# Kernel optimization log

Measured on AMD Instinct MI355X. Metric: run time of the kernel, lower is better.

## Reference

```python
import jax, jax.numpy as jnp
import numpy as np

# Dimensions: SASA-style local self-attention, 7x7 window, 8 groups (heads)
B, CIN, H, W = 4, 256, 64, 64
COUT, K, PAD, STRIDE, DIL, G = 256, 7, 3, 1, 1, 8
CG = COUT // G  # channels per group


def setup_inputs() -> dict:
    key = jax.random.key(0)
    k1, k2, k3, k4, k5, k6 = jax.random.split(key, 6)
    s = 1.0 / np.sqrt(CIN // G)  # fan-in scaling like torch conv init
    return {
        "inputs": jax.random.normal(k1, (B, CIN, H, W), jnp.float32),
        "w_q": jax.random.normal(k2, (G, CG, CIN // G), jnp.float32) * s,
        "w_k": jax.random.normal(k3, (G, CG, CIN // G), jnp.float32) * s,
        "w_v": jax.random.normal(k4, (G, CG, CIN // G), jnp.float32) * s,
        "row_emb": jax.random.normal(k5, (COUT // 2, K), jnp.float32),
        "col_emb": jax.random.normal(k6, (COUT // 2, K), jnp.float32),
    }


def _proj(x, w):
    # grouped 1x1 conv: x [B,CIN,H,W], w [G, CG, CIN/G] -> [B,G,CG,H,W]
    xg = x.reshape(B, G, CIN // G, H, W)
    return jnp.einsum('goc,bgchw->bgohw', w, xg)


def _out_hw():
    ho = (H + 2 * PAD - DIL * (K - 1) - 1) // STRIDE + 1
    wo = (W + 2 * PAD - DIL * (K - 1) - 1) // STRIDE + 1
    return ho, wo


def _patches(x):
    # im2col matching torch.nn.Unfold ordering (kh slow, kw fast)
    # x [B,G,CG,H,W] -> [B,G,CG,K*K,Ho,Wo]
    ho, wo = _out_hw()
    xp = jnp.pad(x, ((0, 0), (0, 0), (0, 0), (PAD, PAD), (PAD, PAD)))
    pats = [
        xp[..., i * DIL: i * DIL + (ho - 1) * STRIDE + 1: STRIDE,
              j * DIL: j * DIL + (wo - 1) * STRIDE + 1: STRIDE]
        for i in range(K) for j in range(K)
    ]
    return jnp.stack(pats, axis=3)


def reference(inputs, w_q, w_k, w_v, row_emb, col_emb):
    ho, wo = _out_hw()
    # queries: 1x1 conv then unfold with kernel 1 / stride -> just strided subsample
    q = _proj(inputs, w_q)[..., ::STRIDE, ::STRIDE]          # [B,G,CG,Ho,Wo]
    kk = _patches(_proj(inputs, w_k))                         # [B,G,CG,K2,Ho,Wo]
    vv = _patches(_proj(inputs, w_v))                         # [B,G,CG,K2,Ho,Wo]
    # relative row/col embeddings, concatenated along channels, split per group
    emb_row = jnp.broadcast_to(row_emb[:, :, None], (COUT // 2, K, K))
    emb_col = jnp.broadcast_to(col_emb[:, None, :], (COUT // 2, K, K))
    emb = jnp.concatenate([emb_row, emb_col], axis=0).reshape(G, CG, K * K)
    # attention logits: per-position dot of query with (key + embedding)
    logits = jnp.einsum('bgchw,bgckhw->bgkhw', q, kk + emb[None, :, :, :, None, None])
    attn = jax.nn.softmax(logits, axis=2)                     # softmax over K*K window
    out = jnp.einsum('bgckhw,bgkhw->bgchw', vv, attn)
    return out.reshape(B, COUT, ho, wo)
```

## Files before the change

kernel.cpp:

```cpp
#include <hip/hip_runtime.h>
#include <hip/hip_bf16.h>
#include <hip/hip_fp16.h>

#define TS   16
#define HS   22
#define HP   484
#define KDW  18
#define KK   7
#define K2   49

typedef _Float16 h2   __attribute__((ext_vector_type(2)));
typedef _Float16 f16x8 __attribute__((ext_vector_type(8)));
typedef float    f32x4 __attribute__((ext_vector_type(4)));
union U32H { unsigned u; h2 h; __half2 p; };

__device__ __forceinline__ h2 pkrtz(float a, float b) {
    auto r = __builtin_amdgcn_cvt_pkrtz(a, b);
    union { decltype(r) i; h2 o; } c; c.i = r;
    return c.o;
}
__device__ __forceinline__ float dot2(h2 a, h2 b, float c) {
#if __has_builtin(__builtin_amdgcn_fdot2)
    return __builtin_amdgcn_fdot2(a, b, c, false);
#else
    return fmaf((float)a.x, (float)b.x, fmaf((float)a.y, (float)b.y, c));
#endif
}
__device__ __forceinline__ float dot2u(unsigned wu, h2 b, float c) {
    U32H w; w.u = wu; return dot2(w.h, b, c);
}
__device__ __forceinline__ float pswap(float v) {
#if __has_builtin(__builtin_amdgcn_mov_dpp)
    int j = __builtin_amdgcn_mov_dpp(__float_as_int(v), 0xB1, 0xF, 0xF, true);
    return __int_as_float(j);
#else
    return __shfl_xor(v, 1, 64);
#endif
}

__global__ __attribute__((amdgpu_flat_work_group_size(512, 512), amdgpu_waves_per_eu(4, 4)))
void sasa_fused_kernel(const float* __restrict__ x,
                       const float* __restrict__ wq,
                       const float* __restrict__ wk,
                       const float* __restrict__ wv,
                       const float* __restrict__ row_emb,
                       const float* __restrict__ col_emb,
                       float* __restrict__ out)
{
    __shared__ h2       s_w[1536];
    __shared__ float    s_emb[224];
    __shared__ unsigned s_ku[HP * KDW];
    __shared__ unsigned s_vu[HP * KDW];

    const int tid = threadIdx.x;

    const int lin  = blockIdx.x + (blockIdx.y << 2) + (blockIdx.z << 4);
    const int xcd  = lin & 7;
    const int slot = lin >> 3;
    const int zg   = xcd + ((slot >> 4) << 3);
    const int sp   = slot & 15;
    const int b    = zg >> 3;
    const int g    = zg & 7;
    const int y0   = (sp >> 2) * TS;
    const int x0   = (sp & 3) * TS;

    const float* xg = x + (size_t)(b * 256 + g * 32) * 4096;

    {
        const int cp  = tid & 15;
        const int cog = tid >> 4;
        const int hh  = cog >> 4;
        const int co  = cog & 15;
        const int di  = (hh * 16 + cp) * 16 + co;
        const float2* wk2 = (const float2*)(wk + g * 1024);
        const float2* wv2 = (const float2*)(wv + g * 1024);
        const float2* wq2 = (const float2*)(wq + g * 1024);
        float2 a = wk2[tid]; s_w[di]        = pkrtz(a.x, a.y);
        float2 v = wv2[tid]; s_w[512 + di]  = pkrtz(v.x, v.y);
        float2 q = wq2[tid]; s_w[1024 + di] = pkrtz(q.x, q.y);
    }
    if (tid < 224) {
        int c = tid / KK, t = tid - c * KK;
        s_emb[tid] = (g < 4) ? row_emb[(g * 32 + c) * KK + t]
                             : col_emb[((g - 4) * 32 + c) * KK + t];
    }
    __syncthreads();

    {
        const int lane = tid & 63;
        const int wid  = tid >> 6;
        const int lrow = lane & 15;
        const int lgrp = lane >> 4;

        f16x8 bk0, bk1, bv0, bv1;
        #pragma unroll
        for (int j = 0; j < 4; ++j) {
            const int cp = lgrp * 4 + j;
            h2 pk0 = s_w[(0 * 16 + cp) * 16 + lrow];
            h2 pk1 = s_w[(1 * 16 + cp) * 16 + lrow];
            h2 pv0 = s_w[512 + (0 * 16 + cp) * 16 + lrow];
            h2 pv1 = s_w[512 + (1 * 16 + cp) * 16 + lrow];
            bk0[2 * j] = pk0.x; bk0[2 * j + 1] = pk0.y;
            bk1[2 * j] = pk1.x; bk1[2 * j + 1] = pk1.y;
            bv0[2 * j] = pv0.x; bv0[2 * j + 1] = pv0.y;
            bv1[2 * j] = pv1.x; bv1[2 * j + 1] = pv1.y;
        }

        _Float16* sk16 = (_Float16*)s_ku;
        _Float16* sv16 = (_Float16*)s_vu;
        const f32x4 zero = {0.f, 0.f, 0.f, 0.f};

        #pragma unroll 1
        for (int t = wid; t < 31; t += 8) {
            const int hp = t * 16 + lrow;
            f16x8 a;
            bool valid = false;
            int gy = 0, gx = 0;
            if (hp < HP) {
                const int hy = hp / HS, hx = hp - hy * HS;
                gy = y0 + hy - 3; gx = x0 + hx - 3;
                valid = ((unsigned)gy < 64u) && ((unsigned)gx < 64u);
            }
            if (valid) {
                const float* xp = xg + gy * 64 + gx + (size_t)(lgrp * 8) * 4096;
                #pragma unroll
                for (int i2 = 0; i2 < 4; ++i2) {
                    h2 pr = pkrtz(xp[(2 * i2) * 4096], xp[(2 * i2 + 1) * 4096]);
                    a[2 * i2] = pr.x; a[2 * i2 + 1] = pr.y;
                }
            } else {
                #pragma unroll
                for (int i = 0; i < 8; ++i) a[i] = (_Float16)0.f;
            }

            f32x4 dk0 = __builtin_amdgcn_mfma_f32_16x16x32_f16(a, bk0, zero, 0, 0, 0);
            f32x4 dk1 = __builtin_amdgcn_mfma_f32_16x16x32_f16(a, bk1, zero, 0, 0, 0);
            f32x4 dv0 = __builtin_amdgcn_mfma_f32_16x16x32_f16(a, bv0, zero, 0, 0, 0);
            f32x4 dv1 = __builtin_amdgcn_mfma_f32_16x16x32_f16(a, bv1, zero, 0, 0, 0);

            #pragma unroll
            for (int r = 0; r < 4; ++r) {
                const int hpo = t * 16 + lgrp * 4 + r;
                if (hpo < HP) {
                    const int base = hpo * 36;
                    sk16[base + lrow]      = (_Float16)dk0[r];
                    sk16[base + 16 + lrow] = (_Float16)dk1[r];
                    sv16[base + lrow]      = (_Float16)dv0[r];
                    sv16[base + 16 + lrow] = (_Float16)dv1[r];
                }
            }
        }
    }

    const int p  = tid >> 1;
    const int h  = tid & 1;
    const int tx = p & 15, ty = p >> 4;
    const int yy = y0 + ty, xx = x0 + tx;
    float accQ[16];
    #pragma unroll
    for (int c = 0; c < 16; ++c) accQ[c] = 0.f;
    {
        const float* xp = xg + yy * 64 + xx;
        h2 xv2[16];
        #pragma unroll
        for (int cp = 0; cp < 16; ++cp)
            xv2[cp] = pkrtz(xp[(2 * cp) * 4096], xp[(2 * cp + 1) * 4096]);
        const h2* wqp = s_w + 1024 + h * 256;
        #pragma unroll
        for (int cp = 0; cp < 16; ++cp) {
            h2 xv = xv2[cp];
            const uint4* wqr = (const uint4*)(wqp + cp * 16);
            uint4 qw[4] = { wqr[0], wqr[1], wqr[2], wqr[3] };
            const unsigned* qwu = (const unsigned*)qw;
            #pragma unroll
            for (int co = 0; co < 16; ++co)
                accQ[co] = dot2u(qwu[co], xv, accQ[co]);
        }
    }

    float qe[KK];
    #pragma unroll
    for (int t = 0; t < KK; ++t) {
        float a = 0.f;
        #pragma unroll
        for (int c = 0; c < 16; ++c)
            a = fmaf(accQ[c], s_emb[(h * 16 + c) * KK + t], a);
        qe[t] = a + 0.f;
    }
    #pragma unroll
    for (int t = 0; t < KK; ++t)
        qe[t] += pswap(qe[t]);

    h2 q2[8];
    #pragma unroll
    for (int j = 0; j < 8; ++j) q2[j] = pkrtz(accQ[2 * j], accQ[2 * j + 1]);

    __syncthreads();

    const int rowsel = (g < 4) ? 1 : 0;

    float lg[K2];
    const unsigned* kb = s_ku + h * 8;
    #pragma unroll
    for (int tp = 0; tp < 24; ++tp) {
        const int t0 = 2 * tp, t1 = t0 + 1;
        const int ki0 = t0 / KK, kj0 = t0 - ki0 * KK;
        const int ki1 = t1 / KK, kj1 = t1 - ki1 * KK;
        const uint2* kp0 = (const uint2*)(kb + ((ty + ki0) * HS + tx + kj0) * KDW);
        const uint2* kp1 = (const uint2*)(kb + ((ty + ki1) * HS + tx + kj1) * KDW);
        uint2 a0 = kp0[0], a1 = kp0[1], a2 = kp0[2], a3 = kp0[3];
        uint2 b0 = kp1[0], b1 = kp1[1], b2 = kp1[2], b3 = kp1[3];
        float p0 = 0.f, p1 = 0.f;
        p0 = dot2u(a0.x, q2[0], p0);  p1 = dot2u(b0.x, q2[0], p1);
        p0 = dot2u(a0.y, q2[1], p0);  p1 = dot2u(b0.y, q2[1], p1);
        p0 = dot2u(a1.x, q2[2], p0);  p1 = dot2u(b1.x, q2[2], p1);
        p0 = dot2u(a1.y, q2[3], p0);  p1 = dot2u(b1.y, q2[3], p1);
        p0 = dot2u(a2.x, q2[4], p0);  p1 = dot2u(b2.x, q2[4], p1);
        p0 = dot2u(a2.y, q2[5], p0);  p1 = dot2u(b2.y, q2[5], p1);
        p0 = dot2u(a3.x, q2[6], p0);  p1 = dot2u(b3.x, q2[6], p1);
        p0 = dot2u(a3.y, q2[7], p0);  p1 = dot2u(b3.y, q2[7], p1);
        lg[t0] = p0 + pswap(p0) + (rowsel ? qe[ki0] : qe[kj0]);
        lg[t1] = p1 + pswap(p1) + (rowsel ? qe[ki1] : qe[kj1]);
    }
    {
        const uint2* kp = (const uint2*)(kb + ((ty + 6) * HS + tx + 6) * KDW);
        uint2 a0 = kp[0], a1 = kp[1], a2 = kp[2], a3 = kp[3];
        float p0 = 0.f;
        p0 = dot2u(a0.x, q2[0], p0); p0 = dot2u(a0.y, q2[1], p0);
        p0 = dot2u(a1.x, q2[2], p0); p0 = dot2u(a1.y, q2[3], p0);
        p0 = dot2u(a2.x, q2[4], p0); p0 = dot2u(a2.y, q2[5], p0);
        p0 = dot2u(a3.x, q2[6], p0); p0 = dot2u(a3.y, q2[7], p0);
        lg[48] = p0 + pswap(p0) + qe[6];
    }

    float m0 = lg[0], m1 = lg[1], m2 = lg[2], m3 = lg[3];
    #pragma unroll
    for (int t = 4; t < 48; t += 4) {
        m0 = fmaxf(m0, lg[t]);
        m1 = fmaxf(m1, lg[t + 1]);
        m2 = fmaxf(m2, lg[t + 2]);
        m3 = fmaxf(m3, lg[t + 3]);
    }
    const float mx = fmaxf(fmaxf(m0, m1), fmaxf(m2, fmaxf(m3, lg[48])));

    float s0 = 0.f, s1 = 0.f, s2 = 0.f, s3 = 0.f;
    #pragma unroll
    for (int t = 0; t < K2; ++t) {
        float pe = __expf(lg[t] - mx);
        lg[t] = pe;
        if ((t & 3) == 0) s0 += pe;
        else if ((t & 3) == 1) s1 += pe;
        else if ((t & 3) == 2) s2 += pe;
        else s3 += pe;
    }
    const float s = (s0 + s1) + (s2 + s3);

    __half2 o2[8];
    #pragma unroll
    for (int j = 0; j < 8; ++j) o2[j] = __float2half2_rn(0.f);

    const unsigned* vb = s_vu + h * 8;
    #pragma unroll
    for (int tp = 0; tp < 24; ++tp) {
        const int t0 = 2 * tp, t1 = t0 + 1;
        const int ki0 = t0 / KK, kj0 = t0 - ki0 * KK;
        const int ki1 = t1 / KK, kj1 = t1 - ki1 * KK;
        const uint2* vp0 = (const uint2*)(vb + ((ty + ki0) * HS + tx + kj0) * KDW);
        const uint2* vp1 = (const uint2*)(vb + ((ty + ki1) * HS + tx + kj1) * KDW);
        uint2 a0 = vp0[0], a1 = vp0[1], a2 = vp0[2], a3 = vp0[3];
        uint2 b0 = vp1[0], b1 = vp1[1], b2 = vp1[2], b3 = vp1[3];
        const __half2 pe0 = __float2half2_rn(lg[t0]);
        const __half2 pe1 = __float2half2_rn(lg[t1]);
        U32H c0, c1, c2, c3, c4, c5, c6, c7;
        c0.u = a0.x; c1.u = a0.y; c2.u = a1.x; c3.u = a1.y;
        c4.u = a2.x; c5.u = a2.y; c6.u = a3.x; c7.u = a3.y;
        o2[0] = __hfma2(c0.p, pe0, o2[0]);
        o2[1] = __hfma2(c1.p, pe0, o2[1]);
        o2[2] = __hfma2(c2.p, pe0, o2[2]);
        o2[3] = __hfma2(c3.p, pe0, o2[3]);
        o2[4] = __hfma2(c4.p, pe0, o2[4]);
        o2[5] = __hfma2(c5.p, pe0, o2[5]);
        o2[6] = __hfma2(c6.p, pe0, o2[6]);
        o2[7] = __hfma2(c7.p, pe0, o2[7]);
        c0.u = b0.x; c1.u = b0.y; c2.u = b1.x; c3.u = b1.y;
        c4.u = b2.x; c5.u = b2.y; c6.u = b3.x; c7.u = b3.y;
        o2[0] = __hfma2(c0.p, pe1, o2[0]);
        o2[1] = __hfma2(c1.p, pe1, o2[1]);
        o2[2] = __hfma2(c2.p, pe1, o2[2]);
        o2[3] = __hfma2(c3.p, pe1, o2[3]);
        o2[4] = __hfma2(c4.p, pe1, o2[4]);
        o2[5] = __hfma2(c5.p, pe1, o2[5]);
        o2[6] = __hfma2(c6.p, pe1, o2[6]);
        o2[7] = __hfma2(c7.p, pe1, o2[7]);
    }
    {
        const uint2* vp = (const uint2*)(vb + ((ty + 6) * HS + tx + 6) * KDW);
        uint2 a0 = vp[0], a1 = vp[1], a2 = vp[2], a3 = vp[3];
        const __half2 pe0 = __float2half2_rn(lg[48]);
        U32H c0, c1, c2, c3, c4, c5, c6, c7;
        c0.u = a0.x; c1.u = a0.y; c2.u = a1.x; c3.u = a1.y;
        c4.u = a2.x; c5.u = a2.y; c6.u = a3.x; c7.u = a3.y;
        o2[0] = __hfma2(c0.p, pe0, o2[0]);
        o2[1] = __hfma2(c1.p, pe0, o2[1]);
        o2[2] = __hfma2(c2.p, pe0, o2[2]);
        o2[3] = __hfma2(c3.p, pe0, o2[3]);
        o2[4] = __hfma2(c4.p, pe0, o2[4]);
        o2[5] = __hfma2(c5.p, pe0, o2[5]);
        o2[6] = __hfma2(c6.p, pe0, o2[6]);
        o2[7] = __hfma2(c7.p, pe0, o2[7]);
    }

    const float inv = 1.0f / s;
    float* op = out + (size_t)(b * 256 + g * 32 + h * 16) * 4096 + yy * 64 + xx;
    #pragma unroll
    for (int j = 0; j < 8; ++j) {
        float2 f = __half22float2(o2[j]);
        op[(2 * j) * 4096]     = f.x * inv;
        op[(2 * j + 1) * 4096] = f.y * inv;
    }
}

extern "C" void kernel_launch(void* const* d_in, const int* in_sizes, int n_in,
                              void* d_out, int out_size, void* d_ws, size_t ws_size,
                              hipStream_t stream) {
    const float* x       = (const float*)d_in[0];
    const float* wq      = (const float*)d_in[1];
    const float* wk      = (const float*)d_in[2];
    const float* wv      = (const float*)d_in[3];
    const float* row_emb = (const float*)d_in[4];
    const float* col_emb = (const float*)d_in[5];
    float* out = (float*)d_out;

    dim3 grid(4, 4, 32);
    dim3 block(512);
    sasa_fused_kernel<<<grid, block, 0, stream>>>(x, wq, wk, wv, row_emb, col_emb, out);
}
```

Measured before the change: 40.06 us.

## Share one LDS buffer for K and V, staging V in registers

Replaces the separate key and value LDS tiles with a single shared buffer. The V projection results are held in registers (packed half2) while logits are computed from K, then written into the same buffer after a barrier, followed by a second barrier before the weighted sum. Halving LDS use, together with relaxing waves_per_eu to 4–8, is meant to let two 512-thread blocks fit per CU. The cost is two extra block-wide barriers and 16 extra live registers per thread across the logit phase.

New measurement: 46.00 us. 14.8% more time.

```diff
diff --git a/kernel.cpp b/kernel.cpp
--- a/kernel.cpp
+++ b/kernel.cpp
@@ -38,7 +38,7 @@
 #endif
 }
 
-__global__ __attribute__((amdgpu_flat_work_group_size(512, 512), amdgpu_waves_per_eu(4, 4)))
+__global__ __attribute__((amdgpu_flat_work_group_size(512, 512), amdgpu_waves_per_eu(4, 8)))
 void sasa_fused_kernel(const float* __restrict__ x,
                        const float* __restrict__ wq,
                        const float* __restrict__ wk,
@@ -49,8 +49,7 @@
 {
     __shared__ h2       s_w[1536];
     __shared__ float    s_emb[224];
-    __shared__ unsigned s_ku[HP * KDW];
-    __shared__ unsigned s_vu[HP * KDW];
+    __shared__ unsigned s_kv[HP * KDW];
 
     const int tid = threadIdx.x;
 
@@ -86,12 +85,13 @@
     }
     __syncthreads();
 
-    {
-        const int lane = tid & 63;
-        const int wid  = tid >> 6;
-        const int lrow = lane & 15;
-        const int lgrp = lane >> 4;
-
+    const int lane = tid & 63;
+    const int wid  = tid >> 6;
+    const int lrow = lane & 15;
+    const int lgrp = lane >> 4;
+    unsigned vv[4][4];
+
+    {
         f16x8 bk0, bk1, bv0, bv1;
         #pragma unroll
         for (int j = 0; j < 4; ++j) {
@@ -106,48 +106,53 @@
             bv1[2 * j] = pv1.x; bv1[2 * j + 1] = pv1.y;
         }
 
-        _Float16* sk16 = (_Float16*)s_ku;
-        _Float16* sv16 = (_Float16*)s_vu;
+        _Float16* sk16 = (_Float16*)s_kv;
         const f32x4 zero = {0.f, 0.f, 0.f, 0.f};
 
-        #pragma unroll 1
-        for (int t = wid; t < 31; t += 8) {
-            const int hp = t * 16 + lrow;
-            f16x8 a;
-            bool valid = false;
-            int gy = 0, gx = 0;
-            if (hp < HP) {
-                const int hy = hp / HS, hx = hp - hy * HS;
-                gy = y0 + hy - 3; gx = x0 + hx - 3;
-                valid = ((unsigned)gy < 64u) && ((unsigned)gx < 64u);
-            }
-            if (valid) {
-                const float* xp = xg + gy * 64 + gx + (size_t)(lgrp * 8) * 4096;
+        #pragma unroll
+        for (int it = 0; it < 4; ++it) {
+            const int t = wid + it * 8;
+            if (t < 31) {
+                const int hp = t * 16 + lrow;
+                f16x8 a;
+                bool valid = false;
+                int gy = 0, gx = 0;
+                if (hp < HP) {
+                    const int hy = hp / HS, hx = hp - hy * HS;
+                    gy = y0 + hy - 3; gx = x0 + hx - 3;
+                    valid = ((unsigned)gy < 64u) && ((unsigned)gx < 64u);
+                }
+                if (valid) {
+                    const float* xp = xg + gy * 64 + gx + (size_t)(lgrp * 8) * 4096;
+                    #pragma unroll
+                    for (int i2 = 0; i2 < 4; ++i2) {
+                        h2 pr = pkrtz(xp[(2 * i2) * 4096], xp[(2 * i2 + 1) * 4096]);
+                        a[2 * i2] = pr.x; a[2 * i2 + 1] = pr.y;
+                    }
+                } else {
+                    #pragma unroll
+                    for (int i = 0; i < 8; ++i) a[i] = (_Float16)0.f;
+                }
+
+                f32x4 dk0 = __builtin_amdgcn_mfma_f32_16x16x32_f16(a, bk0, zero, 0, 0, 0);
+                f32x4 dk1 = __builtin_amdgcn_mfma_f32_16x16x32_f16(a, bk1, zero, 0, 0, 0);
+                f32x4 dv0 = __builtin_amdgcn_mfma_f32_16x16x32_f16(a, bv0, zero, 0, 0, 0);
+                f32x4 dv1 = __builtin_amdgcn_mfma_f32_16x16x32_f16(a, bv1, zero, 0, 0, 0);
+
                 #pragma unroll
-                for (int i2 = 0; i2 < 4; ++i2) {
-                    h2 pr = pkrtz(xp[(2 * i2) * 4096], xp[(2 * i2 + 1) * 4096]);
-                    a[2 * i2] = pr.x; a[2 * i2 + 1] = pr.y;
+                for (int r = 0; r < 4; ++r) {
+                    const int hpo = t * 16 + lgrp * 4 + r;
+                    U32H pv; pv.h = pkrtz(dv0[r], dv1[r]);
+                    vv[it][r] = pv.u;
+                    if (hpo < HP) {
+                        const int base = hpo * 36;
+                        sk16[base + lrow]      = (_Float16)dk0[r];
+                        sk16[base + 16 + lrow] = (_Float16)dk1[r];
+                    }
                 }
             } else {
                 #pragma unroll
-                for (int i = 0; i < 8; ++i) a[i] = (_Float16)0.f;
-            }
-
-            f32x4 dk0 = __builtin_amdgcn_mfma_f32_16x16x32_f16(a, bk0, zero, 0, 0, 0);
-            f32x4 dk1 = __builtin_amdgcn_mfma_f32_16x16x32_f16(a, bk1, zero, 0, 0, 0);
-            f32x4 dv0 = __builtin_amdgcn_mfma_f32_16x16x32_f16(a, bv0, zero, 0, 0, 0);
-            f32x4 dv1 = __builtin_amdgcn_mfma_f32_16x16x32_f16(a, bv1, zero, 0, 0, 0);
-
-            #pragma unroll
-            for (int r = 0; r < 4; ++r) {
-                const int hpo = t * 16 + lgrp * 4 + r;
-                if (hpo < HP) {
-                    const int base = hpo * 36;
-                    sk16[base + lrow]      = (_Float16)dk0[r];
-                    sk16[base + 16 + lrow] = (_Float16)dk1[r];
-                    sv16[base + lrow]      = (_Float16)dv0[r];
-                    sv16[base + 16 + lrow] = (_Float16)dv1[r];
-                }
+                for (int r = 0; r < 4; ++r) vv[it][r] = 0u;
             }
         }
     }
@@ -200,7 +205,7 @@
     const int rowsel = (g < 4) ? 1 : 0;
 
     float lg[K2];
-    const unsigned* kb = s_ku + h * 8;
+    const unsigned* kb = s_kv + h * 8;
     #pragma unroll
     for (int tp = 0; tp < 24; ++tp) {
         const int t0 = 2 * tp, t1 = t0 + 1;
@@ -233,6 +238,27 @@
         lg[48] = p0 + pswap(p0) + qe[6];
     }
 
+    __syncthreads();
+    {
+        _Float16* sv16 = (_Float16*)s_kv;
+        #pragma unroll
+        for (int it = 0; it < 4; ++it) {
+            const int t = wid + it * 8;
+            if (t < 31) {
+                #pragma unroll
+                for (int r = 0; r < 4; ++r) {
+                    const int hpo = t * 16 + lgrp * 4 + r;
+                    if (hpo < HP) {
+                        U32H pv; pv.u = vv[it][r];
+                        const int base = hpo * 36;
+                        sv16[base + lrow]      = pv.h.x;
+                        sv16[base + 16 + lrow] = pv.h.y;
+                    }
+                }
+            }
+        }
+    }
+
     float m0 = lg[0], m1 = lg[1], m2 = lg[2], m3 = lg[3];
     #pragma unroll
     for (int t = 4; t < 48; t += 4) {
@@ -255,11 +281,13 @@
     }
     const float s = (s0 + s1) + (s2 + s3);
 
+    __syncthreads();
+
     __half2 o2[8];
     #pragma unroll
     for (int j = 0; j < 8; ++j) o2[j] = __float2half2_rn(0.f);
 
-    const unsigned* vb = s_vu + h * 8;
+    const unsigned* vb = s_kv + h * 8;
     #pragma unroll
     for (int tp = 0; tp < 24; ++tp) {
         const int t0 = 2 * tp, t1 = t0 + 1;
```
